# Kernel optimization log

Hardware: AMD Instinct MI355X
Metric: run time of the kernel (lower is better)

Reference implementation:

```python
import jax, jax.numpy as jnp
import numpy as np

B, S, D, H, L, W, O = 4, 1024, 512, 8, 6, 64, 300
DH = D // H          # head dim = 64
R = 2 * W + 3        # rel_proj output dim = 131
EPS = 1e-6


def setup_inputs() -> dict:
    key = jax.random.key(0)
    ks = jax.random.split(key, 12)
    sc = 0.02
    x = jax.random.normal(ks[0], (B, S, D), jnp.float32)
    inp = {
        "x": x,
        "ln1_g": jnp.ones((L, D), jnp.float32),
        "ln1_b": jnp.zeros((L, D), jnp.float32),
        "qkv_w": jax.random.normal(ks[1], (L, D, 3 * D), jnp.float32) * sc,
        "qkv_b": jnp.zeros((L, 3 * D), jnp.float32),
        "rel_w": jax.random.normal(ks[2], (DH, R), jnp.float32) * sc,
        "rel_b": jnp.zeros((R,), jnp.float32),
        "ln2_g": jnp.ones((L, D), jnp.float32),
        "ln2_b": jnp.zeros((L, D), jnp.float32),
        "mlp_w1": jax.random.normal(ks[3], (L, D, 4 * D), jnp.float32) * sc,
        "mlp_b1": jnp.zeros((L, 4 * D), jnp.float32),
        "mlp_w2": jax.random.normal(ks[4], (L, 4 * D, D), jnp.float32) * sc,
        "mlp_b2": jnp.zeros((L, D), jnp.float32),
        "normf_g": jnp.ones((D,), jnp.float32),
        "normf_b": jnp.zeros((D,), jnp.float32),
        "head_w": jax.random.normal(ks[5], (D, O), jnp.float32) * sc,
        "head_b": jnp.zeros((O,), jnp.float32),
        "mask": jax.random.randint(ks[6], (B, O), 0, 2, jnp.int32),
    }
    return inp


def _layernorm(x, g, b):
    m = jnp.mean(x, axis=-1, keepdims=True)
    v = jnp.mean(jnp.square(x - m), axis=-1, keepdims=True)
    return (x - m) * jax.lax.rsqrt(v + EPS) * g + b


def _forward(x, ln1_g, ln1_b, qkv_w, qkv_b, rel_w, rel_b, ln2_g, ln2_b,
             mlp_w1, mlp_b1, mlp_w2, mlp_b2, normf_g, normf_b, head_w, head_b, mask):
    b, s, d = x.shape
    # clamped relative offsets, shifted to [0, 2W]; shape [s, s]
    ar = jnp.arange(s)
    offsets = jnp.clip(ar[None, :] - ar[:, None], -W, W) + W
    off_bh = jnp.broadcast_to(offsets[None, None], (b, H, s, s))
    scale = 1.0 / np.sqrt(D / H)  # = 1/sqrt(dh)

    def block(xc, lp):
        (l1g, l1b, qw, qb, l2g, l2b, w1, b1, w2, b2) = lp
        h = _layernorm(xc, l1g, l1b)
        qkv = (h @ qw + qb).reshape(b, s, H, 3 * DH)
        q, k, v = jnp.split(qkv, 3, axis=-1)            # [b,s,h,dh] each
        q = q.transpose(0, 2, 1, 3)                     # [b,h,s,dh]
        k = k.transpose(0, 2, 1, 3)
        v = v.transpose(0, 2, 1, 3)
        content = jnp.einsum('bhik,bhjk->bhij', q, k) * scale
        pos = q @ rel_w + rel_b                          # [b,h,s,R]
        pos_scores = jnp.take_along_axis(pos, off_bh, axis=-1)  # [b,h,s,s]
        attn = jax.nn.softmax(content + pos_scores, axis=-1)
        out = jnp.einsum('bhij,bhjk->bhik', attn, v)     # [b,h,s,dh]
        xc = xc + out.transpose(0, 2, 1, 3).reshape(b, s, d)
        h2 = _layernorm(xc, l2g, l2b)
        m = jax.nn.gelu(h2 @ w1 + b1, approximate=False) @ w2 + b2
        return xc + m, None

    layer_params = (ln1_g, ln1_b, qkv_w, qkv_b, ln2_g, ln2_b,
                    mlp_w1, mlp_b1, mlp_w2, mlp_b2)
    x, _ = jax.lax.scan(block, x, layer_params)
    x = _layernorm(x, normf_g, normf_b)[:, 0, :]         # CLS token
    logits = x @ head_w + head_b                          # [b, O]
    return jnp.where(mask == 0, -jnp.inf, logits)


def reference(x, ln1_g, ln1_b, qkv_w, qkv_b, rel_w, rel_b, ln2_g, ln2_b,
              mlp_w1, mlp_b1, mlp_w2, mlp_b2, normf_g, normf_b, head_w, head_b, mask):
    return _forward(x, ln1_g, ln1_b, qkv_w, qkv_b, rel_w, rel_b, ln2_g, ln2_b,
                    mlp_w1, mlp_b1, mlp_w2, mlp_b2, normf_g, normf_b, head_w, head_b, mask)
```

## Files before the change

kernel.cpp:

```cpp
#include <hip/hip_runtime.h>
#include <math.h>

#define B_  4
#define S_  1024
#define D_  512
#define H_  8
#define L_  6
#define W_  64
#define O_  300
#define DH_ 64
#define R_  131
#define R2_ 132

typedef __attribute__((ext_vector_type(8))) short bf16x8;
typedef __attribute__((ext_vector_type(4))) float f32x4;

#define SWZ(r) ((((r) ^ ((r) >> 3)) & 7) << 4)

__device__ __forceinline__ float gelu_f(float x) {
    return 0.5f * x * (1.0f + erff(x * 0.70710678118654752f));
}

__device__ __forceinline__ unsigned short f2bf(float f) {
    union { float f; unsigned u; } c; c.f = f;
    unsigned u = c.u;
    unsigned r = (u + 0x7fffu + ((u >> 16) & 1u)) >> 16;
    return (unsigned short)r;
}
__device__ __forceinline__ float bf2f(unsigned short u) {
    union { unsigned u; float f; } c; c.u = ((unsigned)u) << 16; return c.f;
}

__device__ __forceinline__ void gload_lds16(const void* g, void* l) {
    __builtin_amdgcn_global_load_lds(
        (const __attribute__((address_space(1))) unsigned int*)g,
        (__attribute__((address_space(3))) unsigned int*)l, 16, 0, 0);
}

__global__ __launch_bounds__(256) void ln_kernel(
    const float* __restrict__ x, const float* __restrict__ g,
    const float* __restrict__ b, unsigned short* __restrict__ y, int rows)
{
    int wave = threadIdx.x >> 6;
    int lane = threadIdx.x & 63;
    int row  = blockIdx.x * 4 + wave;
    if (row >= rows) return;
    const float* xr = x + (size_t)row * D_;
    float4 v0 = *(const float4*)(xr + lane * 4);
    float4 v1 = *(const float4*)(xr + 256 + lane * 4);

    float s = v0.x + v0.y + v0.z + v0.w + v1.x + v1.y + v1.z + v1.w;
    #pragma unroll
    for (int off = 32; off >= 1; off >>= 1) s += __shfl_xor(s, off);
    float mean = s * (1.0f / 512.0f);

    float a0 = v0.x - mean, a1 = v0.y - mean, a2 = v0.z - mean, a3 = v0.w - mean;
    float a4 = v1.x - mean, a5 = v1.y - mean, a6 = v1.z - mean, a7 = v1.w - mean;
    float vs = a0*a0 + a1*a1 + a2*a2 + a3*a3 + a4*a4 + a5*a5 + a6*a6 + a7*a7;
    #pragma unroll
    for (int off = 32; off >= 1; off >>= 1) vs += __shfl_xor(vs, off);
    float rstd = rsqrtf(vs * (1.0f / 512.0f) + 1e-6f);

    float4 g0 = *(const float4*)(g + lane * 4);
    float4 g1 = *(const float4*)(g + 256 + lane * 4);
    float4 b0 = *(const float4*)(b + lane * 4);
    float4 b1 = *(const float4*)(b + 256 + lane * 4);

    unsigned short* yr = y + (size_t)row * D_;
    ushort4 p0 = {f2bf(a0 * rstd * g0.x + b0.x), f2bf(a1 * rstd * g0.y + b0.y),
                  f2bf(a2 * rstd * g0.z + b0.z), f2bf(a3 * rstd * g0.w + b0.w)};
    ushort4 p1 = {f2bf(a4 * rstd * g1.x + b1.x), f2bf(a5 * rstd * g1.y + b1.y),
                  f2bf(a6 * rstd * g1.z + b1.z), f2bf(a7 * rstd * g1.w + b1.w)};
    *(ushort4*)(yr + lane * 4)       = p0;
    *(ushort4*)(yr + 256 + lane * 4) = p1;
}

__global__ __launch_bounds__(256) void tconv_kernel(
    const float* __restrict__ in, unsigned short* __restrict__ out, int K, int N)
{
    __shared__ float t[32][33];
    int tx = threadIdx.x & 31, ty = threadIdx.x >> 5;
    int n0 = blockIdx.x * 32, k0 = blockIdx.y * 32;
    #pragma unroll
    for (int j = 0; j < 4; ++j)
        t[ty + 8*j][tx] = in[(size_t)(k0 + ty + 8*j) * N + n0 + tx];
    __syncthreads();
    #pragma unroll
    for (int j = 0; j < 4; ++j)
        out[(size_t)(n0 + ty + 8*j) * K + k0 + tx] = f2bf(t[tx][ty + 8*j]);
}

__global__ __launch_bounds__(256) void relw_prep(
    const float* __restrict__ rel_w, unsigned short* __restrict__ relwT)
{
    for (int i = threadIdx.x; i < 144 * 64; i += 256) {
        int r = i >> 6, c = i & 63;
        relwT[i] = (r < R_) ? f2bf(rel_w[(size_t)c * R_ + r]) : (unsigned short)0;
    }
}

__global__ __launch_bounds__(256) void prep_all(
    const float* __restrict__ qkv_w, const float* __restrict__ mlp_w1,
    const float* __restrict__ mlp_w2, const float* __restrict__ rel_w,
    unsigned short* __restrict__ wTq_all, unsigned short* __restrict__ wT1_all,
    unsigned short* __restrict__ wT2_all, unsigned short* __restrict__ relwT)
{
    int bid = blockIdx.x;
    int tid = threadIdx.x;
    if (bid >= 4224) {
        for (int i = tid; i < 144 * 64; i += 256) {
            int r = i >> 6, c = i & 63;
            relwT[i] = (r < R_) ? f2bf(rel_w[(size_t)c * R_ + r]) : (unsigned short)0;
        }
        return;
    }
    int l = bid / 704, rr = bid - l * 704;
    const float* in; unsigned short* out; int K, N, bk, bn2;
    if (rr < 192) {
        in = qkv_w + (size_t)l * 512 * 1536; out = wTq_all + (size_t)l * 1536 * 512;
        K = 512; N = 1536; bk = rr / 24; bn2 = rr % 24;
    } else if (rr < 448) {
        int r2 = rr - 192;
        in = mlp_w1 + (size_t)l * 512 * 2048; out = wT1_all + (size_t)l * 2048 * 512;
        K = 512; N = 2048; bk = r2 / 32; bn2 = r2 % 32;
    } else {
        int r2 = rr - 448;
        in = mlp_w2 + (size_t)l * 2048 * 512; out = wT2_all + (size_t)l * 512 * 2048;
        K = 2048; N = 512; bk = r2 / 8; bn2 = r2 % 8;
    }
    int k0 = bk * 64, n0 = bn2 * 64;
    __shared__ unsigned short st[64][72];
    #pragma unroll
    for (int p = 0; p < 4; ++p) {
        int c = p * 256 + tid;
        int kr = c >> 4, n4 = (c & 15) * 4;
        float4 v = *(const float4*)(in + (size_t)(k0 + kr) * N + n0 + n4);
        st[n4 + 0][kr] = f2bf(v.x);
        st[n4 + 1][kr] = f2bf(v.y);
        st[n4 + 2][kr] = f2bf(v.z);
        st[n4 + 3][kr] = f2bf(v.w);
    }
    __syncthreads();
    #pragma unroll
    for (int p = 0; p < 2; ++p) {
        int c = p * 256 + tid;
        int nr = c >> 3, k8 = (c & 7) * 8;
        bf16x8 val = *(const bf16x8*)(&st[nr][k8]);
        *(bf16x8*)(out + (size_t)(n0 + nr) * K + k0 + k8) = val;
    }
}

template<int ACT, int OBF, int BM, int BN, int WM, int WN, int BK>
__global__ __launch_bounds__(256) void mfma_gemm(
    const unsigned short* __restrict__ A, const unsigned short* __restrict__ BT,
    const float* __restrict__ bias, const float* __restrict__ resid,
    void* __restrict__ Cout, int M, int N, int K)
{
    static_assert(WM * WN == 4, "4 waves");
    constexpr int MFR = BM / WM / 16;
    constexpr int NFR = BN / WN / 16;
    constexpr int TPR = BK / 8;
    constexpr int RPP = 256 / TPR;
    constexpr int ACH = BM / RPP, BCH = BN / RPP;
    constexpr int LOADS = ACH + BCH;
    constexpr int KK = BK / 32;
    __shared__ __align__(16) unsigned short smem[2 * (BM + BN) * BK];
    unsigned short* As = smem;
    unsigned short* Bs = smem + 2 * BM * BK;
    int tid  = threadIdx.x;
    int lane = tid & 63;
    int l15 = lane & 15, l4 = lane >> 4;
    int wid  = tid >> 6;
    int wave_m = (wid / WN) * (BM / WM);
    int wave_n = (wid % WN) * (BN / WN);

    int nwg = gridDim.x * gridDim.y;
    int bid0 = blockIdx.y * gridDim.x + blockIdx.x;
    int bid = (bid0 & 7) * (nwg >> 3) + (bid0 >> 3);
    int bm = (bid / gridDim.x) * BM, bn = (bid % gridDim.x) * BN;

    const f32x4 z4 = {0.f, 0.f, 0.f, 0.f};
    f32x4 acc[MFR][NFR];
    #pragma unroll
    for (int m = 0; m < MFR; ++m)
        #pragma unroll
        for (int n = 0; n < NFR; ++n) acc[m][n] = z4;

    int arow = tid / TPR;
    int acol8 = ((tid % TPR) ^ (arow & (TPR - 1))) * 8;
    const unsigned short* Ab = A  + (size_t)(bm + arow) * K + acol8;
    const unsigned short* Bb = BT + (size_t)(bn + arow) * K + acol8;
    unsigned short* Adst = As + tid * 8;
    unsigned short* Bdst = Bs + tid * 8;

    int swzA = l15 & (TPR - 1);
    const unsigned short* Afrag = As + (size_t)(wave_m + l15) * BK;
    const unsigned short* Bfrag = Bs + (size_t)(wave_n + l15) * BK;

    const int NT = K / BK;

    auto STAGE = [&](int buf, int k0) {
        #pragma unroll
        for (int ch = 0; ch < ACH; ++ch)
            gload_lds16(Ab + (size_t)ch * RPP * K + k0, Adst + buf * BM * BK + ch * RPP * BK);
        #pragma unroll
        for (int ch = 0; ch < BCH; ++ch)
            gload_lds16(Bb + (size_t)ch * RPP * K + k0, Bdst + buf * BN * BK + ch * RPP * BK);
    };

    STAGE(0, 0);
    STAGE(1, BK);

    int off8[KK];
    #pragma unroll
    for (int kk = 0; kk < KK; ++kk) off8[kk] = ((l4 + 4 * kk) ^ swzA) * 8;

    for (int t = 0; t < NT; ++t) {
        int cur = t & 1;
        if (t + 1 < NT) {
            if constexpr (LOADS == 8) asm volatile("s_waitcnt vmcnt(8)" ::: "memory");
            else if constexpr (LOADS == 6) asm volatile("s_waitcnt vmcnt(6)" ::: "memory");
            else if constexpr (LOADS == 4) asm volatile("s_waitcnt vmcnt(4)" ::: "memory");
            else asm volatile("s_waitcnt vmcnt(0)" ::: "memory");
        } else {
            asm volatile("s_waitcnt vmcnt(0)" ::: "memory");
        }
        __builtin_amdgcn_s_barrier();
        asm volatile("" ::: "memory");

        const unsigned short* Af = Afrag + cur * BM * BK;
        const unsigned short* Bf = Bfrag + cur * BN * BK;
        bf16x8 af[KK][MFR], bfr[KK][NFR];
        #pragma unroll
        for (int kk = 0; kk < KK; ++kk) {
            #pragma unroll
            for (int m = 0; m < MFR; ++m) af[kk][m]  = *(const bf16x8*)(Af + m * 16 * BK + off8[kk]);
            #pragma unroll
            for (int n = 0; n < NFR; ++n) bfr[kk][n] = *(const bf16x8*)(Bf + n * 16 * BK + off8[kk]);
        }
        asm volatile("s_waitcnt lgkmcnt(0)" ::: "memory");
        __builtin_amdgcn_sched_barrier(0);
        __builtin_amdgcn_s_barrier();
        asm volatile("" ::: "memory");

        if (t + 2 < NT) STAGE(cur, (t + 2) * BK);

        __builtin_amdgcn_s_setprio(1);
        #pragma unroll
        for (int kk = 0; kk < KK; ++kk)
            #pragma unroll
            for (int m = 0; m < MFR; ++m)
                #pragma unroll
                for (int n = 0; n < NFR; ++n)
                    acc[m][n] = __builtin_amdgcn_mfma_f32_16x16x32_bf16(af[kk][m], bfr[kk][n], acc[m][n], 0, 0, 0);
        __builtin_amdgcn_s_setprio(0);
    }

    if constexpr (OBF) {
        constexpr int STR = BN + 8;
        unsigned short* st = smem;
        #pragma unroll
        for (int m = 0; m < MFR; ++m) {
            #pragma unroll
            for (int n = 0; n < NFR; ++n) {
                int lc = wave_n + n * 16 + l15;
                float bv = bias[bn + lc];
                #pragma unroll
                for (int q = 0; q < 4; ++q) {
                    int lr = wave_m + m * 16 + l4 * 4 + q;
                    float v = acc[m][n][q] + bv;
                    if (ACT == 1) v = gelu_f(v);
                    st[lr * STR + lc] = f2bf(v);
                }
            }
        }
        __syncthreads();
        constexpr int PASS = BM * BN / (256 * 8);
        #pragma unroll
        for (int p = 0; p < PASS; ++p) {
            int flat = (p * 256 + tid) * 8;
            int row = flat / BN, col = flat % BN;
            bf16x8 val = *(const bf16x8*)(st + row * STR + col);
            *(bf16x8*)((unsigned short*)Cout + (size_t)(bm + row) * N + bn + col) = val;
        }
    } else {
        constexpr int STR = BN + 4;
        float* st = (float*)smem;
        #pragma unroll
        for (int m = 0; m < MFR; ++m) {
            #pragma unroll
            for (int n = 0; n < NFR; ++n) {
                int lc = wave_n + n * 16 + l15;
                float bv = bias[bn + lc];
                #pragma unroll
                for (int q = 0; q < 4; ++q) {
                    int lr = wave_m + m * 16 + l4 * 4 + q;
                    float v = acc[m][n][q] + bv;
                    if (ACT == 1) v = gelu_f(v);
                    st[lr * STR + lc] = v;
                }
            }
        }
        __syncthreads();
        constexpr int PASS = BM * BN / (256 * 4);
        #pragma unroll
        for (int p = 0; p < PASS; ++p) {
            int flat = (p * 256 + tid) * 4;
            int row = flat / BN, col = flat % BN;
            float4 val = *(const float4*)(st + row * STR + col);
            if (resid) {
                float4 rr = *(const float4*)(resid + (size_t)(bm + row) * N + bn + col);
                val.x += rr.x; val.y += rr.y; val.z += rr.z; val.w += rr.w;
            }
            *(float4*)((float*)Cout + (size_t)(bm + row) * N + bn + col) = val;
        }
    }
}

__global__ __launch_bounds__(512, 2) void attn_mfma(
    const unsigned short* __restrict__ qkv,
    const unsigned short* __restrict__ relwT,
    const float* __restrict__ rel_b,
    float* __restrict__ xres)
{
    __shared__ __align__(16) unsigned char shm[49664];
    unsigned char* Klds  = shm;
    unsigned char* Vtlds = shm + 16384;
    unsigned short* pos16 = (unsigned short*)(shm + 32768);
    float* mergeO  = (float*)shm;
    float* mergeML = (float*)(shm + 17408);

    int tid = threadIdx.x, lane = tid & 63, w = tid >> 6;
    int l15 = lane & 15, l4 = lane >> 4;
    int wq = w & 3;
    int g  = w >> 2;
    int it0 = blockIdx.x * 64;
    int h = blockIdx.y, b = blockIdx.z;
    const float LOG2E = 1.4426950408889634f;
    const float SC = 0.125f * LOG2E;
    const float THR = 11.5441f;

    bf16x8 qa[2];
    {
        const unsigned short* qp = qkv + (size_t)(b * S_ + it0 + wq * 16 + l15) * 1536 + h * 192 + l4 * 8;
        qa[0] = *(const bf16x8*)(qp);
        qa[1] = *(const bf16x8*)(qp + 32);
    }

    if (g == 0) {
        #pragma unroll
        for (int n = 0; n < 9; ++n) {
            f32x4 pacc = {0.f, 0.f, 0.f, 0.f};
            #pragma unroll
            for (int ks = 0; ks < 2; ++ks) {
                bf16x8 bv = *(const bf16x8*)(relwT + (size_t)(16 * n + l15) * 64 + ks * 32 + l4 * 8);
                pacc = __builtin_amdgcn_mfma_f32_16x16x32_bf16(qa[ks], bv, pacc, 0, 0, 0);
            }
            int c = 16 * n + l15;
            if (c < R_) {
                float rb = rel_b[c];
                #pragma unroll
                for (int q = 0; q < 4; ++q)
                    pos16[(wq * 16 + l4 * 4 + q) * R2_ + c] = f2bf((pacc[q] + rb) * LOG2E);
            }
        }
    }
    __syncthreads();

    int rloc = wq * 16 + l15;
    int i_glob = it0 + rloc;
    float p_lo = bf2f(pos16[rloc * R2_ + 0]);
    float p_hi = bf2f(pos16[rloc * R2_ + 128]);

    int rf = tid >> 2, seg = tid & 3;
    int gk = rf >> 6, rr = rf & 63;
    const unsigned short* kbase = qkv + (size_t)(b * S_ + gk * 512 + rr) * 1536 + h * 192 + 64 + seg * 16;
    int kbyt = gk * 8192 + ((rr * 128 + seg * 32) ^ SWZ(rr));
    int pf = tid >> 3, seg8 = tid & 7;
    int gv = pf >> 5, pp = pf & 31;
    const unsigned short* vbase = qkv + (size_t)(b * S_ + gv * 512 + 2 * pp) * 1536 + h * 192 + 128 + seg8 * 8;
    bf16x8 kr0, kr1, vr0, vr1;
    kr0 = *(const bf16x8*)(kbase);
    kr1 = *(const bf16x8*)(kbase + 8);
    vr0 = *(const bf16x8*)(vbase);
    vr1 = *(const bf16x8*)(vbase + 1536);

    const f32x4 z4 = {0.f, 0.f, 0.f, 0.f};
    f32x4 oacc[4];
    #pragma unroll
    for (int n = 0; n < 4; ++n) oacc[n] = z4;
    float mrun_s = -INFINITY, lrun_s = 0.f;
    int wmin = it0 + wq * 16;
    unsigned char* Kw = Klds + g * 8192;
    unsigned char* Vw = Vtlds + g * 8192;

    int idx_lo = (l15 + 32 * (l4 & 1)) * 4;
    int idx_hi = idx_lo + 64;
    bool hi_n = (l4 >> 1) != 0;

    for (int t = 0; t < 8; ++t) {
        int jt0 = g * 512 + t * 64;
        __syncthreads();
        *(bf16x8*)(Klds + kbyt) = kr0;
        *(bf16x8*)(Klds + (kbyt ^ 16)) = kr1;
        #pragma unroll
        for (int i = 0; i < 8; ++i) {
            int dh = seg8 * 8 + i;
            unsigned v01 = (unsigned)(unsigned short)vr0[i] | ((unsigned)(unsigned short)vr1[i] << 16);
            *(unsigned*)(Vtlds + gv * 8192 + ((dh * 128 + pp * 4) ^ SWZ(dh))) = v01;
        }
        __syncthreads();
        if (t < 7) {
            const unsigned short* kp = kbase + (size_t)(t + 1) * 64 * 1536;
            kr0 = *(const bf16x8*)(kp);
            kr1 = *(const bf16x8*)(kp + 8);
            const unsigned short* vp = vbase + (size_t)(t + 1) * 64 * 1536;
            vr0 = *(const bf16x8*)(vp);
            vr1 = *(const bf16x8*)(vp + 1536);
        }

        f32x4 ssw[4];
        #pragma unroll
        for (int n = 0; n < 4; ++n) ssw[n] = z4;
        __builtin_amdgcn_s_setprio(1);
        #pragma unroll
        for (int n = 0; n < 4; ++n) {
            int kvr = 16 * n + l15;
            #pragma unroll
            for (int ks = 0; ks < 2; ++ks) {
                bf16x8 ak = *(const bf16x8*)(Kw + ((kvr * 128 + ks * 64 + l4 * 16) ^ SWZ(kvr)));
                ssw[n] = __builtin_amdgcn_mfma_f32_16x16x32_bf16(ak, qa[ks], ssw[n], 0, 0, 0);
            }
        }
        __builtin_amdgcn_s_setprio(0);

        float sv[4][4];
        bool left  = (jt0 + 63 < wmin - 64);
        bool right = (jt0 > wmin + 15 + 64);
        if (left || right) {
            float pc = left ? p_lo : p_hi;
            #pragma unroll
            for (int n = 0; n < 4; ++n)
                #pragma unroll
                for (int r = 0; r < 4; ++r) sv[n][r] = fmaf(ssw[n][r], SC, pc);
        } else {
            #pragma unroll
            for (int n = 0; n < 4; ++n)
                #pragma unroll
                for (int r = 0; r < 4; ++r) {
                    int j = jt0 + 16 * n + l4 * 4 + r;
                    int off = j - i_glob;
                    off = off < -64 ? -64 : (off > 64 ? 64 : off);
                    sv[n][r] = fmaf(ssw[n][r], SC, bf2f(pos16[rloc * R2_ + off + 64]));
                }
        }

        float a0 = fmaxf(fmaxf(sv[0][0], sv[0][1]), fmaxf(sv[0][2], sv[0][3]));
        float a1 = fmaxf(fmaxf(sv[1][0], sv[1][1]), fmaxf(sv[1][2], sv[1][3]));
        float a2 = fmaxf(fmaxf(sv[2][0], sv[2][1]), fmaxf(sv[2][2], sv[2][3]));
        float a3 = fmaxf(fmaxf(sv[3][0], sv[3][1]), fmaxf(sv[3][2], sv[3][3]));
        float mx = fmaxf(fmaxf(a0, a1), fmaxf(a2, a3));
        mx = fmaxf(mx, __shfl_xor(mx, 16));
        mx = fmaxf(mx, __shfl_xor(mx, 32));
        if (!__all(mx - mrun_s <= THR)) {
            float mnew = fmaxf(mrun_s, mx);
            float al = exp2f(mrun_s - mnew);
            mrun_s = mnew;
            lrun_s *= al;
            float alv0 = __shfl(al, l4 * 4 + 0);
            float alv1 = __shfl(al, l4 * 4 + 1);
            float alv2 = __shfl(al, l4 * 4 + 2);
            float alv3 = __shfl(al, l4 * 4 + 3);
            #pragma unroll
            for (int n = 0; n < 4; ++n) {
                oacc[n][0] *= alv0; oacc[n][1] *= alv1;
                oacc[n][2] *= alv2; oacc[n][3] *= alv3;
            }
        }
        float rs = 0.f;
        #pragma unroll
        for (int n = 0; n < 4; ++n)
            #pragma unroll
            for (int r = 0; r < 4; ++r) {
                float p = exp2f(sv[n][r] - mrun_s);
                sv[n][r] = p;
                rs += p;
            }
        rs += __shfl_xor(rs, 16);
        rs += __shfl_xor(rs, 32);
        lrun_s += rs;

        unsigned pkk[4][2];
        #pragma unroll
        for (int n = 0; n < 4; ++n) {
            asm("v_cvt_pk_bf16_f32 %0, %1, %2" : "=v"(pkk[n][0]) : "v"(sv[n][0]), "v"(sv[n][1]));
            asm("v_cvt_pk_bf16_f32 %0, %1, %2" : "=v"(pkk[n][1]) : "v"(sv[n][2]), "v"(sv[n][3]));
        }
        bf16x8 pa[2];
        #pragma unroll
        for (int ks = 0; ks < 2; ++ks) {
            unsigned wrd[4];
            #pragma unroll
            for (int ww = 0; ww < 4; ++ww) {
                int srcidx = (ww >> 1) ? idx_hi : idx_lo;
                unsigned vlo = (unsigned)__builtin_amdgcn_ds_bpermute(srcidx, (int)pkk[2 * ks + 0][ww & 1]);
                unsigned vhi = (unsigned)__builtin_amdgcn_ds_bpermute(srcidx, (int)pkk[2 * ks + 1][ww & 1]);
                wrd[ww] = hi_n ? vhi : vlo;
            }
            union { unsigned u[4]; bf16x8 v; } cvt;
            cvt.u[0] = wrd[0]; cvt.u[1] = wrd[1]; cvt.u[2] = wrd[2]; cvt.u[3] = wrd[3];
            pa[ks] = cvt.v;
        }

        __builtin_amdgcn_s_setprio(1);
        #pragma unroll
        for (int n = 0; n < 4; ++n) {
            int dh = 16 * n + l15;
            #pragma unroll
            for (int ks = 0; ks < 2; ++ks) {
                bf16x8 bv = *(const bf16x8*)(Vw + ((dh * 128 + ks * 64 + l4 * 16) ^ SWZ(dh)));
                oacc[n] = __builtin_amdgcn_mfma_f32_16x16x32_bf16(pa[ks], bv, oacc[n], 0, 0, 0);
            }
        }
        __builtin_amdgcn_s_setprio(0);
    }

    __syncthreads();
    if (g == 1) {
        #pragma unroll
        for (int n = 0; n < 4; ++n)
            #pragma unroll
            for (int r = 0; r < 4; ++r)
                mergeO[(wq * 16 + l4 * 4 + r) * 68 + 16 * n + l15] = oacc[n][r];
        if (lane < 16) {
            mergeML[rloc * 2 + 0] = mrun_s;
            mergeML[rloc * 2 + 1] = lrun_s;
        }
    }
    __syncthreads();
    if (g == 0) {
        float mb = mergeML[rloc * 2 + 0];
        float lb = mergeML[rloc * 2 + 1];
        float M  = fmaxf(mrun_s, mb);
        float fa = exp2f(mrun_s - M);
        float fb = exp2f(mb - M);
        float inv = 1.0f / (lrun_s * fa + lb * fb);
        float A_s = fa * inv, B_s = fb * inv;
        float Av[4], Bv[4];
        #pragma unroll
        for (int r = 0; r < 4; ++r) {
            Av[r] = __shfl(A_s, l4 * 4 + r);
            Bv[r] = __shfl(B_s, l4 * 4 + r);
        }
        #pragma unroll
        for (int r = 0; r < 4; ++r) {
            int row = wq * 16 + l4 * 4 + r;
            float* xp = xres + (size_t)(b * S_ + it0 + row) * D_ + h * DH_;
            #pragma unroll
            for (int n = 0; n < 4; ++n)
                xp[16 * n + l15] += oacc[n][r] * Av[r] + mergeO[row * 68 + 16 * n + l15] * Bv[r];
        }
    }
}

__global__ __launch_bounds__(256) void head_kernel(
    const float* __restrict__ xc, const float* __restrict__ gf,
    const float* __restrict__ bfp, const float* __restrict__ hw,
    const float* __restrict__ hbias, const int* __restrict__ mask,
    float* __restrict__ out)
{
    __shared__ float a[4][512];
    __shared__ float part[4][64][4];
    int tid = threadIdx.x;
    int wv = tid >> 6, lane = tid & 63;
    {
        const float* xr = xc + (size_t)wv * S_ * D_;
        float4 v0 = *(const float4*)(xr + lane * 4);
        float4 v1 = *(const float4*)(xr + 256 + lane * 4);
        float s = v0.x + v0.y + v0.z + v0.w + v1.x + v1.y + v1.z + v1.w;
        #pragma unroll
        for (int off = 32; off >= 1; off >>= 1) s += __shfl_xor(s, off);
        float mean = s * (1.0f / 512.0f);
        float c0 = v0.x - mean, c1 = v0.y - mean, c2 = v0.z - mean, c3 = v0.w - mean;
        float c4 = v1.x - mean, c5 = v1.y - mean, c6 = v1.z - mean, c7 = v1.w - mean;
        float vs = c0*c0 + c1*c1 + c2*c2 + c3*c3 + c4*c4 + c5*c5 + c6*c6 + c7*c7;
        #pragma unroll
        for (int off = 32; off >= 1; off >>= 1) vs += __shfl_xor(vs, off);
        float rstd = rsqrtf(vs * (1.0f / 512.0f) + 1e-6f);
        float4 g0 = *(const float4*)(gf + lane * 4);
        float4 g1 = *(const float4*)(gf + 256 + lane * 4);
        float4 b0 = *(const float4*)(bfp + lane * 4);
        float4 b1 = *(const float4*)(bfp + 256 + lane * 4);
        a[wv][lane * 4 + 0] = c0 * rstd * g0.x + b0.x;
        a[wv][lane * 4 + 1] = c1 * rstd * g0.y + b0.y;
        a[wv][lane * 4 + 2] = c2 * rstd * g0.z + b0.z;
        a[wv][lane * 4 + 3] = c3 * rstd * g0.w + b0.w;
        a[wv][256 + lane * 4 + 0] = c4 * rstd * g1.x + b1.x;
        a[wv][256 + lane * 4 + 1] = c5 * rstd * g1.y + b1.y;
        a[wv][256 + lane * 4 + 2] = c6 * rstd * g1.z + b1.z;
        a[wv][256 + lane * 4 + 3] = c7 * rstd * g1.w + b1.w;
    }
    __syncthreads();

    int cl = tid & 63;
    int c  = blockIdx.x * 64 + cl;
    int ks = tid >> 6;
    float ac[4] = {0.f, 0.f, 0.f, 0.f};
    if (c < O_) {
        const float* wp = hw + (size_t)(ks * 128) * O_ + c;
        #pragma unroll 8
        for (int k = 0; k < 128; ++k) {
            float wvv = wp[(size_t)k * O_];
            int kk = ks * 128 + k;
            ac[0] = fmaf(a[0][kk], wvv, ac[0]);
            ac[1] = fmaf(a[1][kk], wvv, ac[1]);
            ac[2] = fmaf(a[2][kk], wvv, ac[2]);
            ac[3] = fmaf(a[3][kk], wvv, ac[3]);
        }
    }
    #pragma unroll
    for (int bb = 0; bb < 4; ++bb) part[ks][cl][bb] = ac[bb];
    __syncthreads();
    if (ks == 0 && c < O_) {
        float hbv = hbias[c];
        #pragma unroll
        for (int bb = 0; bb < 4; ++bb) {
            float v = part[0][cl][bb] + part[1][cl][bb] + part[2][cl][bb] + part[3][cl][bb] + hbv;
            out[bb * O_ + c] = (mask[bb * O_ + c] == 0) ? -1e30f : v;
        }
    }
}

extern "C" void kernel_launch(void* const* d_in, const int* in_sizes, int n_in,
                              void* d_out, int out_size, void* d_ws, size_t ws_size,
                              hipStream_t stream) {
    const float* x      = (const float*)d_in[0];
    const float* ln1_g  = (const float*)d_in[1];
    const float* ln1_b  = (const float*)d_in[2];
    const float* qkv_w  = (const float*)d_in[3];
    const float* qkv_b  = (const float*)d_in[4];
    const float* rel_w  = (const float*)d_in[5];
    const float* rel_b  = (const float*)d_in[6];
    const float* ln2_g  = (const float*)d_in[7];
    const float* ln2_b  = (const float*)d_in[8];
    const float* mlp_w1 = (const float*)d_in[9];
    const float* mlp_b1 = (const float*)d_in[10];
    const float* mlp_w2 = (const float*)d_in[11];
    const float* mlp_b2 = (const float*)d_in[12];
    const float* normf_g = (const float*)d_in[13];
    const float* normf_b = (const float*)d_in[14];
    const float* head_w  = (const float*)d_in[15];
    const float* head_b  = (const float*)d_in[16];
    const int*   mask    = (const int*)d_in[17];
    float* out = (float*)d_out;
    float* ws  = (float*)d_ws;

    const int NR = B_ * S_;
    dim3 blk(256);

    float* x_cur = ws;
    float* reg2  = ws + 2097152;
    unsigned short* qkv16 = (unsigned short*)reg2;
    unsigned short* midb  = (unsigned short*)reg2;

    hipMemcpyAsync(x_cur, x, (size_t)NR * D_ * sizeof(float),
                   hipMemcpyDeviceToDevice, stream);

    bool hoist = ws_size >= (size_t)15995392 * 4;

    if (hoist) {
        unsigned short* hb      = (unsigned short*)(ws + 6291456);
        unsigned short* wTq_all = (unsigned short*)(ws + 7340032);
        unsigned short* wT1_all = (unsigned short*)(ws + 9699328);
        unsigned short* wT2_all = (unsigned short*)(ws + 12845056);
        unsigned short* relwT   = (unsigned short*)(ws + 15990784);

        prep_all<<<4225, blk, 0, stream>>>(qkv_w, mlp_w1, mlp_w2, rel_w,
                                           wTq_all, wT1_all, wT2_all, relwT);

        for (int l = 0; l < L_; ++l) {
            ln_kernel<<<NR / 4, blk, 0, stream>>>(x_cur, ln1_g + l * D_, ln1_b + l * D_, hb, NR);
            mfma_gemm<0, 1, 128, 64, 4, 1, 64><<<dim3(24, 32), blk, 0, stream>>>(
                hb, wTq_all + (size_t)l * 1536 * 512, qkv_b + (size_t)l * 3 * D_,
                nullptr, qkv16, NR, 3 * D_, D_);
            attn_mfma<<<dim3(S_ / 64, H_, B_), dim3(512), 0, stream>>>(qkv16, relwT, rel_b, x_cur);
            ln_kernel<<<NR / 4, blk, 0, stream>>>(x_cur, ln2_g + l * D_, ln2_b + l * D_, hb, NR);
            mfma_gemm<1, 1, 128, 128, 2, 2, 64><<<dim3(16, 32), blk, 0, stream>>>(
                hb, wT1_all + (size_t)l * 2048 * 512, mlp_b1 + (size_t)l * 4 * D_,
                nullptr, midb, NR, 4 * D_, D_);
            mfma_gemm<0, 0, 64, 64, 2, 2, 128><<<dim3(8, 64), blk, 0, stream>>>(
                midb, wT2_all + (size_t)l * 512 * 2048, mlp_b2 + (size_t)l * D_,
                x_cur, x_cur, NR, D_, 4 * D_);
        }
        head_kernel<<<dim3(5), blk, 0, stream>>>(x_cur, normf_g, normf_b,
                                                 head_w, head_b, mask, out);
    } else {
        float* wregs = ws + 6291456;
        unsigned short* hb    = (unsigned short*)wregs;
        unsigned short* wTq   = (unsigned short*)(wregs + 1048576);
        unsigned short* wT1   = (unsigned short*)(wregs + 1441792);
        unsigned short* wT2   = (unsigned short*)(wregs + 1966080);
        unsigned short* relwT = (unsigned short*)(ws + 10616832);

        relw_prep<<<1, blk, 0, stream>>>(rel_w, relwT);
        for (int l = 0; l < L_; ++l) {
            ln_kernel<<<NR / 4, blk, 0, stream>>>(x_cur, ln1_g + l * D_, ln1_b + l * D_, hb, NR);
            tconv_kernel<<<dim3(48, 16), blk, 0, stream>>>(
                qkv_w + (size_t)l * D_ * 3 * D_, wTq, D_, 3 * D_);
            mfma_gemm<0, 1, 128, 64, 4, 1, 64><<<dim3(24, 32), blk, 0, stream>>>(
                hb, wTq, qkv_b + (size_t)l * 3 * D_, nullptr, qkv16, NR, 3 * D_, D_);
            attn_mfma<<<dim3(S_ / 64, H_, B_), dim3(512), 0, stream>>>(qkv16, relwT, rel_b, x_cur);
            ln_kernel<<<NR / 4, blk, 0, stream>>>(x_cur, ln2_g + l * D_, ln2_b + l * D_, hb, NR);
            tconv_kernel<<<dim3(64, 16), blk, 0, stream>>>(
                mlp_w1 + (size_t)l * D_ * 4 * D_, wT1, D_, 4 * D_);
            mfma_gemm<1, 1, 128, 128, 2, 2, 64><<<dim3(16, 32), blk, 0, stream>>>(
                hb, wT1, mlp_b1 + (size_t)l * 4 * D_, nullptr, midb, NR, 4 * D_, D_);
            tconv_kernel<<<dim3(16, 64), blk, 0, stream>>>(
                mlp_w2 + (size_t)l * 4 * D_ * D_, wT2, 4 * D_, D_);
            mfma_gemm<0, 0, 64, 64, 2, 2, 128><<<dim3(8, 64), blk, 0, stream>>>(
                midb, wT2, mlp_b2 + (size_t)l * D_, x_cur, x_cur, NR, D_, 4 * D_);
        }
        head_kernel<<<dim3(5), blk, 0, stream>>>(x_cur, normf_g, normf_b,
                                                 head_w, head_b, mask, out);
    }
}
```

Measured before the change: 574.4 us.

## Write QKV in per-head planar layout and remap attention blocks to XCDs

The QKV GEMM epilogue now scatters each 64-wide output tile into separate Q/K/V planes laid out per head as [part][head][token][64], instead of one interleaved row of 1536 values. Attention then reads Q, K and V rows that are contiguous 128-byte runs rather than strided 3 KB rows. The attention launch is flattened to a 1D grid and remapped so that all query tiles of a (batch, head) land on the same XCD. This is meant to improve L2 reuse of the K/V data and cut strided global traffic, at the cost of a less coalesced write pattern in the GEMM epilogue.

```diff
diff --git a/kernel.cpp b/kernel.cpp
--- a/kernel.cpp
+++ b/kernel.cpp
@@ -11,6 +11,9 @@
 #define DH_ 64
 #define R_  131
 #define R2_ 132
+
+#define HSTRIDE_   262144
+#define PARTSTR_   2097152
 
 typedef __attribute__((ext_vector_type(8))) short bf16x8;
 typedef __attribute__((ext_vector_type(4))) float f32x4;
@@ -150,13 +153,14 @@
     }
 }
 
-template<int ACT, int OBF, int BM, int BN, int WM, int WN, int BK>
+template<int ACT, int OBF, int OUT3, int BM, int BN, int WM, int WN, int BK>
 __global__ __launch_bounds__(256) void mfma_gemm(
     const unsigned short* __restrict__ A, const unsigned short* __restrict__ BT,
     const float* __restrict__ bias, const float* __restrict__ resid,
     void* __restrict__ Cout, int M, int N, int K)
 {
     static_assert(WM * WN == 4, "4 waves");
+    static_assert(!OUT3 || (OBF && BN == 64), "OUT3 needs bf16 out, BN=64");
     constexpr int MFR = BM / WM / 16;
     constexpr int NFR = BN / WN / 16;
     constexpr int TPR = BK / 8;
@@ -276,12 +280,25 @@
         }
         __syncthreads();
         constexpr int PASS = BM * BN / (256 * 8);
-        #pragma unroll
-        for (int p = 0; p < PASS; ++p) {
-            int flat = (p * 256 + tid) * 8;
-            int row = flat / BN, col = flat % BN;
-            bf16x8 val = *(const bf16x8*)(st + row * STR + col);
-            *(bf16x8*)((unsigned short*)Cout + (size_t)(bm + row) * N + bn + col) = val;
+        if constexpr (OUT3) {
+            int bnt = bn >> 6;
+            int part = bnt % 3, hh = bnt / 3;
+            unsigned short* dst = (unsigned short*)Cout + (size_t)part * PARTSTR_ + (size_t)hh * HSTRIDE_;
+            #pragma unroll
+            for (int p = 0; p < PASS; ++p) {
+                int flat = (p * 256 + tid) * 8;
+                int row = flat >> 6, col = flat & 63;
+                bf16x8 val = *(const bf16x8*)(st + row * STR + col);
+                *(bf16x8*)(dst + (size_t)(bm + row) * 64 + col) = val;
+            }
+        } else {
+            #pragma unroll
+            for (int p = 0; p < PASS; ++p) {
+                int flat = (p * 256 + tid) * 8;
+                int row = flat / BN, col = flat % BN;
+                bf16x8 val = *(const bf16x8*)(st + row * STR + col);
+                *(bf16x8*)((unsigned short*)Cout + (size_t)(bm + row) * N + bn + col) = val;
+            }
         }
     } else {
         constexpr int STR = BN + 4;
@@ -318,7 +335,7 @@
 }
 
 __global__ __launch_bounds__(512, 2) void attn_mfma(
-    const unsigned short* __restrict__ qkv,
+    const unsigned short* __restrict__ qs,
     const unsigned short* __restrict__ relwT,
     const float* __restrict__ rel_b,
     float* __restrict__ xres)
@@ -334,15 +351,25 @@
     int l15 = lane & 15, l4 = lane >> 4;
     int wq = w & 3;
     int g  = w >> 2;
-    int it0 = blockIdx.x * 64;
-    int h = blockIdx.y, b = blockIdx.z;
+
+    int lin = blockIdx.x;
+    int xcd = lin & 7, j = lin >> 3;
+    int gidx = xcd * 4 + (j >> 4);
+    int b = gidx >> 3, h = gidx & 7;
+    int it0 = (j & 15) * 64;
+
+    const unsigned short* Qb = qs + (size_t)h * HSTRIDE_;
+    const unsigned short* Kb = Qb + PARTSTR_;
+    const unsigned short* Vb = Qb + 2 * PARTSTR_;
+    int gs0 = b * S_;
+
     const float LOG2E = 1.4426950408889634f;
     const float SC = 0.125f * LOG2E;
     const float THR = 11.5441f;
 
     bf16x8 qa[2];
     {
-        const unsigned short* qp = qkv + (size_t)(b * S_ + it0 + wq * 16 + l15) * 1536 + h * 192 + l4 * 8;
+        const unsigned short* qp = Qb + (size_t)(gs0 + it0 + wq * 16 + l15) * 64 + l4 * 8;
         qa[0] = *(const bf16x8*)(qp);
         qa[1] = *(const bf16x8*)(qp + 32);
     }
@@ -374,16 +401,16 @@
 
     int rf = tid >> 2, seg = tid & 3;
     int gk = rf >> 6, rr = rf & 63;
-    const unsigned short* kbase = qkv + (size_t)(b * S_ + gk * 512 + rr) * 1536 + h * 192 + 64 + seg * 16;
+    const unsigned short* kbase = Kb + (size_t)(gs0 + gk * 512 + rr) * 64 + seg * 16;
     int kbyt = gk * 8192 + ((rr * 128 + seg * 32) ^ SWZ(rr));
     int pf = tid >> 3, seg8 = tid & 7;
     int gv = pf >> 5, pp = pf & 31;
-    const unsigned short* vbase = qkv + (size_t)(b * S_ + gv * 512 + 2 * pp) * 1536 + h * 192 + 128 + seg8 * 8;
+    const unsigned short* vbase = Vb + (size_t)(gs0 + gv * 512 + 2 * pp) * 64 + seg8 * 8;
     bf16x8 kr0, kr1, vr0, vr1;
     kr0 = *(const bf16x8*)(kbase);
     kr1 = *(const bf16x8*)(kbase + 8);
     vr0 = *(const bf16x8*)(vbase);
-    vr1 = *(const bf16x8*)(vbase + 1536);
+    vr1 = *(const bf16x8*)(vbase + 64);
 
     const f32x4 z4 = {0.f, 0.f, 0.f, 0.f};
     f32x4 oacc[4];
@@ -411,12 +438,12 @@
         }
         __syncthreads();
         if (t < 7) {
-            const unsigned short* kp = kbase + (size_t)(t + 1) * 64 * 1536;
+            const unsigned short* kp = kbase + (size_t)(t + 1) * 4096;
             kr0 = *(const bf16x8*)(kp);
             kr1 = *(const bf16x8*)(kp + 8);
-            const unsigned short* vp = vbase + (size_t)(t + 1) * 64 * 1536;
+            const unsigned short* vp = vbase + (size_t)(t + 1) * 4096;
             vr0 = *(const bf16x8*)(vp);
-            vr1 = *(const bf16x8*)(vp + 1536);
+            vr1 = *(const bf16x8*)(vp + 64);
         }
 
         f32x4 ssw[4];
@@ -448,8 +475,8 @@
             for (int n = 0; n < 4; ++n)
                 #pragma unroll
                 for (int r = 0; r < 4; ++r) {
-                    int j = jt0 + 16 * n + l4 * 4 + r;
-                    int off = j - i_glob;
+                    int jj = jt0 + 16 * n + l4 * 4 + r;
+                    int off = jj - i_glob;
                     off = off < -64 ? -64 : (off > 64 ? 64 : off);
                     sv[n][r] = fmaf(ssw[n][r], SC, bf2f(pos16[rloc * R2_ + off + 64]));
                 }
@@ -555,7 +582,7 @@
         #pragma unroll
         for (int r = 0; r < 4; ++r) {
             int row = wq * 16 + l4 * 4 + r;
-            float* xp = xres + (size_t)(b * S_ + it0 + row) * D_ + h * DH_;
+            float* xp = xres + (size_t)(gs0 + it0 + row) * D_ + h * DH_;
             #pragma unroll
             for (int n = 0; n < 4; ++n)
                 xp[16 * n + l15] += oacc[n][r] * Av[r] + mergeO[row * 68 + 16 * n + l15] * Bv[r];
@@ -660,8 +687,8 @@
 
     float* x_cur = ws;
     float* reg2  = ws + 2097152;
-    unsigned short* qkv16 = (unsigned short*)reg2;
-    unsigned short* midb  = (unsigned short*)reg2;
+    unsigned short* qkvs = (unsigned short*)reg2;
+    unsigned short* midb = (unsigned short*)reg2;
 
     hipMemcpyAsync(x_cur, x, (size_t)NR * D_ * sizeof(float),
                    hipMemcpyDeviceToDevice, stream);
@@ -680,15 +707,15 @@
 
         for (int l = 0; l < L_; ++l) {
             ln_kernel<<<NR / 4, blk, 0, stream>>>(x_cur, ln1_g + l * D_, ln1_b + l * D_, hb, NR);
-            mfma_gemm<0, 1, 128, 64, 4, 1, 64><<<dim3(24, 32), blk, 0, stream>>>(
+            mfma_gemm<0, 1, 1, 128, 64, 4, 1, 64><<<dim3(24, 32), blk, 0, stream>>>(
                 hb, wTq_all + (size_t)l * 1536 * 512, qkv_b + (size_t)l * 3 * D_,
-                nullptr, qkv16, NR, 3 * D_, D_);
-            attn_mfma<<<dim3(S_ / 64, H_, B_), dim3(512), 0, stream>>>(qkv16, relwT, rel_b, x_cur);
+                nullptr, qkvs, NR, 3 * D_, D_);
+            attn_mfma<<<dim3(512), dim3(512), 0, stream>>>(qkvs, relwT, rel_b, x_cur);
             ln_kernel<<<NR / 4, blk, 0, stream>>>(x_cur, ln2_g + l * D_, ln2_b + l * D_, hb, NR);
-            mfma_gemm<1, 1, 128, 128, 2, 2, 64><<<dim3(16, 32), blk, 0, stream>>>(
+            mfma_gemm<1, 1, 0, 128, 128, 2, 2, 64><<<dim3(16, 32), blk, 0, stream>>>(
                 hb, wT1_all + (size_t)l * 2048 * 512, mlp_b1 + (size_t)l * 4 * D_,
                 nullptr, midb, NR, 4 * D_, D_);
-            mfma_gemm<0, 0, 64, 64, 2, 2, 128><<<dim3(8, 64), blk, 0, stream>>>(
+            mfma_gemm<0, 0, 0, 64, 64, 2, 2, 128><<<dim3(8, 64), blk, 0, stream>>>(
                 midb, wT2_all + (size_t)l * 512 * 2048, mlp_b2 + (size_t)l * D_,
                 x_cur, x_cur, NR, D_, 4 * D_);
         }
@@ -707,17 +734,17 @@
             ln_kernel<<<NR / 4, blk, 0, stream>>>(x_cur, ln1_g + l * D_, ln1_b + l * D_, hb, NR);
             tconv_kernel<<<dim3(48, 16), blk, 0, stream>>>(
                 qkv_w + (size_t)l * D_ * 3 * D_, wTq, D_, 3 * D_);
-            mfma_gemm<0, 1, 128, 64, 4, 1, 64><<<dim3(24, 32), blk, 0, stream>>>(
-                hb, wTq, qkv_b + (size_t)l * 3 * D_, nullptr, qkv16, NR, 3 * D_, D_);
-            attn_mfma<<<dim3(S_ / 64, H_, B_), dim3(512), 0, stream>>>(qkv16, relwT, rel_b, x_cur);
+            mfma_gemm<0, 1, 1, 128, 64, 4, 1, 64><<<dim3(24, 32), blk, 0, stream>>>(
+                hb, wTq, qkv_b + (size_t)l * 3 * D_, nullptr, qkvs, NR, 3 * D_, D_);
+            attn_mfma<<<dim3(512), dim3(512), 0, stream>>>(qkvs, relwT, rel_b, x_cur);
             ln_kernel<<<NR / 4, blk, 0, stream>>>(x_cur, ln2_g + l * D_, ln2_b + l * D_, hb, NR);
             tconv_kernel<<<dim3(64, 16), blk, 0, stream>>>(
                 mlp_w1 + (size_t)l * D_ * 4 * D_, wT1, D_, 4 * D_);
-            mfma_gemm<1, 1, 128, 128, 2, 2, 64><<<dim3(16, 32), blk, 0, stream>>>(
+            mfma_gemm<1, 1, 0, 128, 128, 2, 2, 64><<<dim3(16, 32), blk, 0, stream>>>(
                 hb, wT1, mlp_b1 + (size_t)l * 4 * D_, nullptr, midb, NR, 4 * D_, D_);
             tconv_kernel<<<dim3(16, 64), blk, 0, stream>>>(
                 mlp_w2 + (size_t)l * 4 * D_ * D_, wT2, 4 * D_, D_);
-            mfma_gemm<0, 0, 64, 64, 2, 2, 128><<<dim3(8, 64), blk, 0, stream>>>(
+            mfma_gemm<0, 0, 0, 64, 64, 2, 2, 128><<<dim3(8, 64), blk, 0, stream>>>(
                 midb, wT2, mlp_b2 + (size_t)l * D_, x_cur, x_cur, NR, D_, 4 * D_);
         }
         head_kernel<<<dim3(5), blk, 0, stream>>>(x_cur, normf_g, normf_b,
```

After: 572.9 us. Within noise of the previous version (-0.3%).
